# Kernel tuning notes

Hardware: AMD Instinct MI355X
Metric: run time of the kernel (lower is better)

The kernel has to match this reference:

```python
import jax, jax.numpy as jnp
import numpy as np

DIM = 33  # LUT lattice size per axis


def setup_inputs() -> dict:
    key = jax.random.key(0)
    k1, k2 = jax.random.split(key)
    # Learned parameter (initialized to zeros in the module; random here so the
    # output is non-trivial for correctness checking).
    LUT = jax.random.normal(k1, (3, DIM, DIM, DIM), dtype=jnp.float32) * 0.1
    # Input image batch, pixel values in [0, 1)
    x = jax.random.uniform(k2, (8, 3, 1024, 1024), dtype=jnp.float32)
    return {"LUT": LUT, "x": x}


def trilinear_lut(LUT, x):
    """Per-pixel trilinear interpolation over a 3D color LUT.

    LUT: (3, dim, dim, dim), indexed [channel, b_bin, g_bin, r_bin]
         (matches the CUDA kernel's flat index r + g*dim + b*dim^2).
    x:   (B, 3, H, W) RGB in [0, 1].
    Returns (B, 3, H, W).
    """
    dim = LUT.shape[1]
    binsize = 1.0 / (dim - 1)
    r, g, b = x[:, 0], x[:, 1], x[:, 2]  # each (B, H, W)
    rf, gf, bf = r / binsize, g / binsize, b / binsize
    # bin indices, clipped so id+1 stays in range (handles x == 1.0)
    rid = jnp.clip(jnp.floor(rf).astype(jnp.int32), 0, dim - 2)
    gid = jnp.clip(jnp.floor(gf).astype(jnp.int32), 0, dim - 2)
    bid = jnp.clip(jnp.floor(bf).astype(jnp.int32), 0, dim - 2)
    # fractional offsets within the cell
    rd = rf - rid
    gd = gf - gid
    bd = bf - bid

    out = jnp.zeros((3,) + r.shape, dtype=x.dtype)  # (3, B, H, W)
    for db in (0, 1):
        wb = bd if db else (1.0 - bd)
        for dg in (0, 1):
            wg = gd if dg else (1.0 - gd)
            for dr in (0, 1):
                wr = rd if dr else (1.0 - rd)
                w = wr * wg * wb                      # (B, H, W)
                v = LUT[:, bid + db, gid + dg, rid + dr]  # gather -> (3, B, H, W)
                out = out + w[None] * v
    return jnp.transpose(out, (1, 0, 2, 3))  # (B, 3, H, W)


def reference(LUT, x):
    return trilinear_lut(LUT, x)
```

## Files before the change

kernel.cpp:

```cpp
#include <hip/hip_runtime.h>

#define DIM  33
#define DIM2 (DIM * DIM)
#define DIM3 (DIM * DIM * DIM)

typedef float  f32x4 __attribute__((ext_vector_type(4)));
typedef unsigned int u32x4 __attribute__((ext_vector_type(4)));

struct RGB { float r, g, b; };

__device__ __forceinline__ unsigned int q10(float v) {
    int q = (int)rintf(v * 512.0f);
    q = min(max(q, -512), 511);
    return (unsigned int)(q & 0x3FF);
}

__global__ void pack_lut_kernel(const float* __restrict__ lut, unsigned int* __restrict__ t) {
    int i = blockIdx.x * blockDim.x + threadIdx.x;
    if (i >= DIM3) return;
    t[i] = q10(lut[i]) | (q10(lut[i + DIM3]) << 10) | (q10(lut[i + 2 * DIM3]) << 20);
}

__device__ __forceinline__ float bfe10(unsigned int w, int bit) {
    return (float)((int)(w << (22 - bit)) >> 22);
}

__device__ __forceinline__ RGB interp_pixel(const unsigned int* lut_s,
                                            float r, float g, float b) {
    float rf = r * 32.0f, gf = g * 32.0f, bf = b * 32.0f;
    int rid = min(max((int)rf, 0), 31);
    int gid = min(max((int)gf, 0), 31);
    int bid = min(max((int)bf, 0), 31);
    float rd = rf - (float)rid, gd = gf - (float)gid, bd = bf - (float)bid;
    float rd1 = 1.0f - rd, gd1 = 1.0f - gd;

    int idx = rid + DIM * gid + DIM2 * bid;
    unsigned int c000 = lut_s[idx];
    unsigned int c100 = lut_s[idx + 1];
    unsigned int c010 = lut_s[idx + DIM];
    unsigned int c110 = lut_s[idx + DIM + 1];
    unsigned int c001 = lut_s[idx + DIM2];
    unsigned int c101 = lut_s[idx + DIM2 + 1];
    unsigned int c011 = lut_s[idx + DIM2 + DIM];
    unsigned int c111 = lut_s[idx + DIM2 + DIM + 1];

    float bl = (1.0f - bd) * (1.0f / 512.0f);
    float bh = bd * (1.0f / 512.0f);
    float w00 = rd1 * gd1, w10 = rd * gd1, w01 = rd1 * gd, w11 = rd * gd;
    float w000 = w00 * bl, w100 = w10 * bl, w010 = w01 * bl, w110 = w11 * bl;
    float w001 = w00 * bh, w101 = w10 * bh, w011 = w01 * bh, w111 = w11 * bh;

    RGB o;
    o.r = w000 * bfe10(c000, 0)  + w100 * bfe10(c100, 0)  + w010 * bfe10(c010, 0)  + w110 * bfe10(c110, 0)
        + w001 * bfe10(c001, 0)  + w101 * bfe10(c101, 0)  + w011 * bfe10(c011, 0)  + w111 * bfe10(c111, 0);
    o.g = w000 * bfe10(c000, 10) + w100 * bfe10(c100, 10) + w010 * bfe10(c010, 10) + w110 * bfe10(c110, 10)
        + w001 * bfe10(c001, 10) + w101 * bfe10(c101, 10) + w011 * bfe10(c011, 10) + w111 * bfe10(c111, 10);
    o.b = w000 * bfe10(c000, 20) + w100 * bfe10(c100, 20) + w010 * bfe10(c010, 20) + w110 * bfe10(c110, 20)
        + w001 * bfe10(c001, 20) + w101 * bfe10(c101, 20) + w011 * bfe10(c011, 20) + w111 * bfe10(c111, 20);
    return o;
}

__global__ void __launch_bounds__(1024, 4) lut_apply_kernel(
    const unsigned int* __restrict__ t,
    const float* __restrict__ x,
    float* __restrict__ out)
{
    __shared__ __align__(16) unsigned int lut_s[DIM3];
    {
        const u32x4* t4 = reinterpret_cast<const u32x4*>(t);
        u32x4* s4 = reinterpret_cast<u32x4*>(lut_s);
        for (int i = threadIdx.x; i < DIM3 / 4; i += 1024)
            s4[i] = t4[i];
        if (threadIdx.x == 0) lut_s[DIM3 - 1] = t[DIM3 - 1];
    }
    __syncthreads();

    const int PLANE = 1024 * 1024;
    const int NQ_PER_IMG = PLANE / 4;
    const int STRIDE = 512 * 1024;

    int tid = blockIdx.x * 1024 + threadIdx.x;

    size_t bases[4];
    f32x4 rv[4], gv[4], bv[4];
#pragma unroll
    for (int k = 0; k < 4; ++k) {
        int q = tid + k * STRIDE;
        int img = q >> 18;
        int p = q & (NQ_PER_IMG - 1);
        size_t base = (size_t)img * 3 * PLANE + (size_t)p * 4;
        bases[k] = base;
        rv[k] = __builtin_nontemporal_load(reinterpret_cast<const f32x4*>(x + base));
        gv[k] = __builtin_nontemporal_load(reinterpret_cast<const f32x4*>(x + base + PLANE));
        bv[k] = __builtin_nontemporal_load(reinterpret_cast<const f32x4*>(x + base + 2 * PLANE));
    }

#pragma unroll
    for (int k = 0; k < 4; ++k) {
        RGB p0 = interp_pixel(lut_s, rv[k].x, gv[k].x, bv[k].x);
        RGB p1 = interp_pixel(lut_s, rv[k].y, gv[k].y, bv[k].y);
        RGB p2 = interp_pixel(lut_s, rv[k].z, gv[k].z, bv[k].z);
        RGB p3 = interp_pixel(lut_s, rv[k].w, gv[k].w, bv[k].w);

        f32x4 orv = { p0.r, p1.r, p2.r, p3.r };
        f32x4 ogv = { p0.g, p1.g, p2.g, p3.g };
        f32x4 obv = { p0.b, p1.b, p2.b, p3.b };

        size_t base = bases[k];
        *reinterpret_cast<f32x4*>(out + base) = orv;
        *reinterpret_cast<f32x4*>(out + base + PLANE) = ogv;
        *reinterpret_cast<f32x4*>(out + base + 2 * PLANE) = obv;
    }
}

extern "C" void kernel_launch(void* const* d_in, const int* in_sizes, int n_in,
                              void* d_out, int out_size, void* d_ws, size_t ws_size,
                              hipStream_t stream) {
    const float* lut = (const float*)d_in[0];
    const float* x   = (const float*)d_in[1];
    float* out = (float*)d_out;

    unsigned int* t = (unsigned int*)d_ws;

    pack_lut_kernel<<<(DIM3 + 255) / 256, 256, 0, stream>>>(lut, t);

    lut_apply_kernel<<<512, 1024, 0, stream>>>(t, x, out);

    (void)in_sizes; (void)n_in; (void)out_size; (void)ws_size;
}
```

Before: 52.95 us.

## Halve grid and software-pipeline input loads two chunks ahead

The grid drops from 512 to 256 blocks and each thread now handles 8 chunks of 4 pixels instead of 4. Loads for chunk j+2 are issued before chunk j is interpolated, and a sched_barrier stops the compiler from reordering across iterations. This spreads the cost of filling the LUT into shared memory over more work and overlaps global loads with LDS gathers and math. In exchange there are fewer blocks, which can leave CUs idle (256 blocks across 256 CUs), and register pressure rises from holding three chunks of inputs at once.

```diff
diff --git a/kernel.cpp b/kernel.cpp
--- a/kernel.cpp
+++ b/kernel.cpp
@@ -77,40 +77,50 @@
 
     const int PLANE = 1024 * 1024;
     const int NQ_PER_IMG = PLANE / 4;
-    const int STRIDE = 512 * 1024;
+    const int STRIDE = 256 * 1024;
+    const int NCH = 8;
 
     int tid = blockIdx.x * 1024 + threadIdx.x;
 
-    size_t bases[4];
-    f32x4 rv[4], gv[4], bv[4];
-#pragma unroll
-    for (int k = 0; k < 4; ++k) {
-        int q = tid + k * STRIDE;
-        int img = q >> 18;
-        int p = q & (NQ_PER_IMG - 1);
-        size_t base = (size_t)img * 3 * PLANE + (size_t)p * 4;
-        bases[k] = base;
-        rv[k] = __builtin_nontemporal_load(reinterpret_cast<const f32x4*>(x + base));
-        gv[k] = __builtin_nontemporal_load(reinterpret_cast<const f32x4*>(x + base + PLANE));
-        bv[k] = __builtin_nontemporal_load(reinterpret_cast<const f32x4*>(x + base + 2 * PLANE));
-    }
+#define BASEOF(k) ({ int _q = tid + (k) * STRIDE;                          \
+                     int _img = _q >> 18;                                  \
+                     int _p = _q & (NQ_PER_IMG - 1);                       \
+                     (size_t)_img * 3 * PLANE + (size_t)_p * 4; })
+
+    f32x4 R[NCH], G[NCH], B[NCH];
+
+#define LOADC(k) do {                                                                  \
+        size_t _b = BASEOF(k);                                                         \
+        R[k] = __builtin_nontemporal_load(reinterpret_cast<const f32x4*>(x + _b));     \
+        G[k] = __builtin_nontemporal_load(reinterpret_cast<const f32x4*>(x + _b + PLANE)); \
+        B[k] = __builtin_nontemporal_load(reinterpret_cast<const f32x4*>(x + _b + 2 * PLANE)); \
+    } while (0)
+
+    LOADC(0);
+    LOADC(1);
 
 #pragma unroll
-    for (int k = 0; k < 4; ++k) {
-        RGB p0 = interp_pixel(lut_s, rv[k].x, gv[k].x, bv[k].x);
-        RGB p1 = interp_pixel(lut_s, rv[k].y, gv[k].y, bv[k].y);
-        RGB p2 = interp_pixel(lut_s, rv[k].z, gv[k].z, bv[k].z);
-        RGB p3 = interp_pixel(lut_s, rv[k].w, gv[k].w, bv[k].w);
+    for (int j = 0; j < NCH; ++j) {
+        if (j + 2 < NCH) LOADC(j + 2);
+
+        RGB p0 = interp_pixel(lut_s, R[j].x, G[j].x, B[j].x);
+        RGB p1 = interp_pixel(lut_s, R[j].y, G[j].y, B[j].y);
+        RGB p2 = interp_pixel(lut_s, R[j].z, G[j].z, B[j].z);
+        RGB p3 = interp_pixel(lut_s, R[j].w, G[j].w, B[j].w);
 
         f32x4 orv = { p0.r, p1.r, p2.r, p3.r };
         f32x4 ogv = { p0.g, p1.g, p2.g, p3.g };
         f32x4 obv = { p0.b, p1.b, p2.b, p3.b };
 
-        size_t base = bases[k];
+        size_t base = BASEOF(j);
         *reinterpret_cast<f32x4*>(out + base) = orv;
         *reinterpret_cast<f32x4*>(out + base + PLANE) = ogv;
         *reinterpret_cast<f32x4*>(out + base + 2 * PLANE) = obv;
+
+        __builtin_amdgcn_sched_barrier(0);
     }
+#undef LOADC
+#undef BASEOF
 }
 
 extern "C" void kernel_launch(void* const* d_in, const int* in_sizes, int n_in,
@@ -124,7 +134,7 @@
 
     pack_lut_kernel<<<(DIM3 + 255) / 256, 256, 0, stream>>>(lut, t);
 
-    lut_apply_kernel<<<512, 1024, 0, stream>>>(t, x, out);
+    lut_apply_kernel<<<256, 1024, 0, stream>>>(t, x, out);
 
     (void)in_sizes; (void)n_in; (void)out_size; (void)ws_size;
 }
```

Result: faster. 46.06 us (-13.0%).
